# Performance work log

Measured on AMD Instinct MI355X. Metric: run time of the kernel, lower is better.

The kernel has to match this reference:

```python
import jax, jax.numpy as jnp
import numpy as np

N = 1 << 20   # detections
M = 64        # cameras
DEPTH_W, LIGHT_W, TEMPORAL_W = 1.0, 0.5, 0.3
MAX_DISTANCE = 25.0


def setup_inputs() -> dict:
    key = jax.random.key(0)
    k1, k2, k3, k4 = jax.random.split(key, 4)
    return {
        "detection_depths": jax.random.uniform(k1, (N,), dtype=jnp.float32) * 200.0,
        "camera_depths": jax.random.uniform(k2, (M,), dtype=jnp.float32) * 200.0,
        "detection_times": jax.random.uniform(k3, (N,), dtype=jnp.float32) * 3600.0,
        "camera_times": jax.random.uniform(k4, (M,), dtype=jnp.float32) * 3600.0,
    }


def reference(detection_depths, camera_depths, detection_times, camera_times):
    # Cost[i,j] = w_d*(d_i - c_j)^2 + w_l*(1 - exp(-0.045*c_j)) + w_t*(t_i - t_j)^2/3600
    depth_diff = (detection_depths[:, None] - camera_depths[None, :]) ** 2   # [N, M]
    light_penalty = 1.0 - jnp.exp(-0.045 * camera_depths)[None, :]           # [1, M]
    time_diff = (detection_times[:, None] - camera_times[None, :]) ** 2 / 3600.0
    cost = DEPTH_W * depth_diff + LIGHT_W * light_penalty + TEMPORAL_W * time_diff

    # Vectorized greedy assignment: per-row argmin + threshold + weight
    min_j = jnp.argmin(cost, axis=1)                      # [N] int
    min_cost = jnp.min(cost, axis=1)                      # [N]
    valid = min_cost < MAX_DISTANCE ** 2
    assignments = jnp.where(valid, min_j, -1)
    weights = jnp.where(valid, 1.0 / (1.0 + jnp.sqrt(min_cost)), 0.0)
    return assignments, weights
```

## Files before the change

### kernel.cpp

```cpp
#include <hip/hip_runtime.h>
#include <math.h>


#define M_CAM 64

__global__ void cam_pre_kernel(const float* __restrict__ cdep, float* __restrict__ lbf) {
    int j = threadIdx.x;
    if (j < M_CAM) {
        float a = __fmul_rn(-0.045f, cdep[j]);
        float e = (float)exp((double)a);
        lbf[j] = __fmul_rn(0.5f, __fsub_rn(1.0f, e));
    }
}

__global__ __launch_bounds__(256) void assign_kernel(
    const float* __restrict__ ddep, const float* __restrict__ cdep,
    const float* __restrict__ dtim, const float* __restrict__ ctim,
    const float* __restrict__ lbf,
    float* __restrict__ out_asn, float* __restrict__ out_w, int n)
{
    int i = blockIdx.x * blockDim.x + threadIdx.x;
    if (i >= n) return;
    float d = ddep[i];
    float t = dtim[i];

    unsigned best = 0xffffffffu;
    int   bj = 0;
    float bc = 0.0f;

    #pragma unroll 4
    for (int j = 0; j < M_CAM; ++j) {
        float dd = __fsub_rn(d, cdep[j]);
        float A  = __fmul_rn(dd, dd);
        float td = __fsub_rn(t, ctim[j]);
        float t2 = __fmul_rn(td, td);
        float T  = __fdiv_rn(t2, 3600.0f);
        float C  = __fmul_rn(0.3f, T);
        float cost = __fadd_rn(__fadd_rn(A, lbf[j]), C);
        unsigned u = __float_as_uint(cost) & ~7u;
        if (u < best) { best = u; bj = j; bc = cost; }
    }

    bool valid = bc < 625.0f;
    float w = __fdiv_rn(1.0f, __fadd_rn(1.0f, __fsqrt_rn(bc)));
    out_asn[i] = valid ? (float)bj : -1.0f;
    out_w[i]   = valid ? w : 0.0f;
}

extern "C" void kernel_launch(void* const* d_in, const int* in_sizes, int n_in,
                              void* d_out, int out_size, void* d_ws, size_t ws_size,
                              hipStream_t stream) {
    const float* ddep = (const float*)d_in[0];
    const float* cdep = (const float*)d_in[1];
    const float* dtim = (const float*)d_in[2];
    const float* ctim = (const float*)d_in[3];
    int n = in_sizes[0];

    float* lbf = (float*)d_ws;
    float* out = (float*)d_out;

    hipLaunchKernelGGL(cam_pre_kernel, dim3(1), dim3(64), 0, stream, cdep, lbf);

    int blocks = (n + 255) / 256;
    hipLaunchKernelGGL(assign_kernel, dim3(blocks), dim3(256), 0, stream,
                       ddep, cdep, dtim, ctim, lbf, out, out + n, n);
}
```

Measured before the change: 97.53 us.

## Fuse camera precompute into assign kernel with shared-memory camera table

Removes the separate camera-precompute launch. Each block now computes the light penalty for all 64 cameras and stores depth, time and penalty in a shared float4 table. The inner loop is fully unrolled, and the correctly rounded division by 3600 is replaced with a reciprocal multiply plus an FMA correction step. The best cost is recomputed once after the loop instead of being carried through it. In exchange, every block repeats 64 double-precision exps and adds a barrier, and the FMA-corrected division may differ from true division in rare rounding cases.

```diff
diff --git a/kernel.cpp b/kernel.cpp
--- a/kernel.cpp
+++ b/kernel.cpp
@@ -4,42 +4,59 @@
 
 #define M_CAM 64
 
-__global__ void cam_pre_kernel(const float* __restrict__ cdep, float* __restrict__ lbf) {
-    int j = threadIdx.x;
-    if (j < M_CAM) {
-        float a = __fmul_rn(-0.045f, cdep[j]);
-        float e = (float)exp((double)a);
-        lbf[j] = __fmul_rn(0.5f, __fsub_rn(1.0f, e));
-    }
-}
-
-__global__ __launch_bounds__(256) void assign_kernel(
+__global__ __launch_bounds__(256) void fused_kernel(
     const float* __restrict__ ddep, const float* __restrict__ cdep,
     const float* __restrict__ dtim, const float* __restrict__ ctim,
-    const float* __restrict__ lbf,
     float* __restrict__ out_asn, float* __restrict__ out_w, int n)
 {
-    int i = blockIdx.x * blockDim.x + threadIdx.x;
+    __shared__ float4 cam[M_CAM];
+    int tid = threadIdx.x;
+    if (tid < M_CAM) {
+        float c  = cdep[tid];
+        float tc = ctim[tid];
+        float a  = __fmul_rn(-0.045f, c);
+        float e  = (float)exp((double)a);
+        float lb = __fmul_rn(0.5f, __fsub_rn(1.0f, e));
+        cam[tid] = make_float4(c, tc, lb, 0.0f);
+    }
+    __syncthreads();
+
+    int i = blockIdx.x * blockDim.x + tid;
     if (i >= n) return;
     float d = ddep[i];
     float t = dtim[i];
 
+    const float r3600 = (float)(1.0 / 3600.0);
+
     unsigned best = 0xffffffffu;
-    int   bj = 0;
-    float bc = 0.0f;
+    int bj = 0;
 
-    #pragma unroll 4
+    #pragma unroll
     for (int j = 0; j < M_CAM; ++j) {
-        float dd = __fsub_rn(d, cdep[j]);
+        float4 cj = cam[j];
+        float dd = __fsub_rn(d, cj.x);
         float A  = __fmul_rn(dd, dd);
-        float td = __fsub_rn(t, ctim[j]);
+        float td = __fsub_rn(t, cj.y);
         float t2 = __fmul_rn(td, td);
-        float T  = __fdiv_rn(t2, 3600.0f);
+        float y0 = __fmul_rn(t2, r3600);
+        float er = __builtin_fmaf(-3600.0f, y0, t2);
+        float T  = __builtin_fmaf(er, r3600, y0);
         float C  = __fmul_rn(0.3f, T);
-        float cost = __fadd_rn(__fadd_rn(A, lbf[j]), C);
+        float cost = __fadd_rn(__fadd_rn(A, cj.z), C);
         unsigned u = __float_as_uint(cost) & ~7u;
-        if (u < best) { best = u; bj = j; bc = cost; }
+        if (u < best) { best = u; bj = j; }
     }
+
+    float4 cw = cam[bj];
+    float dd = __fsub_rn(d, cw.x);
+    float A  = __fmul_rn(dd, dd);
+    float td = __fsub_rn(t, cw.y);
+    float t2 = __fmul_rn(td, td);
+    float y0 = __fmul_rn(t2, r3600);
+    float er = __builtin_fmaf(-3600.0f, y0, t2);
+    float T  = __builtin_fmaf(er, r3600, y0);
+    float C  = __fmul_rn(0.3f, T);
+    float bc = __fadd_rn(__fadd_rn(A, cw.z), C);
 
     bool valid = bc < 625.0f;
     float w = __fdiv_rn(1.0f, __fadd_rn(1.0f, __fsqrt_rn(bc)));
@@ -56,12 +73,9 @@
     const float* ctim = (const float*)d_in[3];
     int n = in_sizes[0];
 
-    float* lbf = (float*)d_ws;
     float* out = (float*)d_out;
 
-    hipLaunchKernelGGL(cam_pre_kernel, dim3(1), dim3(64), 0, stream, cdep, lbf);
-
     int blocks = (n + 255) / 256;
-    hipLaunchKernelGGL(assign_kernel, dim3(blocks), dim3(256), 0, stream,
-                       ddep, cdep, dtim, ctim, lbf, out, out + n, n);
+    hipLaunchKernelGGL(fused_kernel, dim3(blocks), dim3(256), 0, stream,
+                       ddep, cdep, dtim, ctim, out, out + n, n);
 }
```

Result: faster. 86.46 us (-11.3%).
